# Kernel tuning notes

Hardware: AMD Instinct MI355X
Metric: run time of the kernel (lower is better)

## Reference

```python
import jax, jax.numpy as jnp
import numpy as np

SCOPE = 27
RICKER_WIDTH = 6.0
DAMPING = 0.12
IN_CHANNELS = 256


def _ricker(scope, std, damping):
    # mexican-hat / ricker wavelet, length `scope`, centered
    x = jnp.arange(scope, dtype=jnp.float32) - (scope // 2)
    a = 2.0 / (jnp.sqrt(3.0 * std) * jnp.pi ** 0.25)
    return damping * a * (1.0 - (x / std) ** 2) * jnp.exp(-(x ** 2) / (2.0 * std ** 2))


def _pad_roll(k, in_channels):
    # zero-pad kernel (length scope) to in_channels, roll so center sits at i=0-ish
    scope = k.shape[-1]
    pad_left = (in_channels - scope) // 2
    pad_right = in_channels - scope - pad_left
    padded = jnp.concatenate([jnp.zeros((pad_left,), k.dtype), k, jnp.zeros((pad_right,), k.dtype)])
    return jnp.roll(padded, in_channels // 2 + 1)


def _circulant(kernel, c):
    # tpl[i, j] = kernel[(j - i) mod C]  (each row is the kernel rolled by i)
    idx = (jnp.arange(c)[None, :] - jnp.arange(c)[:, None]) % c
    return kernel[idx]


def setup_inputs() -> dict:
    key = jax.random.key(0)
    k1, _ = jax.random.split(key)
    activations = jax.random.normal(k1, (32, IN_CHANNELS, 64, 64), dtype=jnp.float32)
    inhibition_filter = _ricker(SCOPE, RICKER_WIDTH, DAMPING)  # learned param, ricker init
    return {"activations": activations, "inhibition_filter": inhibition_filter}


def reference(activations, inhibition_filter):
    n, c, h, w = activations.shape
    kernel = _pad_roll(inhibition_filter, c)              # [C]
    tpl = _circulant(kernel, c)                           # [C, C]
    tpl_inv = jnp.linalg.inv(jnp.eye(c, dtype=tpl.dtype) - tpl)  # [C, C]
    # torch: (N, H*W, C) @ tpl_inv -> out[n, c_out, h, w] = sum_k act[n, k, h, w] * tpl_inv[k, c_out]
    return jnp.einsum('nkhw,kc->nchw', activations, tpl_inv)
```

## Files before the change

kernel.cpp:

```cpp
#include <hip/hip_runtime.h>
#include <hip/hip_bf16.h>

#define C 256
#define HW 4096
#define CHUNK_STRIDE 66

typedef __attribute__((ext_vector_type(8))) short short8;
typedef __attribute__((ext_vector_type(4))) float float4v;

__device__ __forceinline__ unsigned short f2bf(float x) {
    unsigned u = __builtin_bit_cast(unsigned, x);
    u = (u + 0x7fffu + ((u >> 16) & 1u)) >> 16;
    return (unsigned short)u;
}

__device__ __forceinline__ void g2l_b32(const void* g, void* l) {
    __builtin_amdgcn_global_load_lds(
        (const __attribute__((address_space(1))) unsigned int*)g,
        (__attribute__((address_space(3))) unsigned int*)l, 4, 0, 0);
}
__device__ __forceinline__ void g2l_b128(const void* g, void* l) {
    __builtin_amdgcn_global_load_lds(
        (const __attribute__((address_space(1))) unsigned int*)g,
        (__attribute__((address_space(3))) unsigned int*)l, 16, 0, 0);
}

__global__ void build_tab_kernel(const float* __restrict__ filt, unsigned short* __restrict__ tab) {
    __shared__ float twc[256], tws[256];
    __shared__ float Gre[256], Gim[256];
    __shared__ float gsh[256];
    const int t = threadIdx.x;
    const double PI = 3.14159265358979323846;
    double th = (double)t * (PI / 128.0);
    twc[t] = (float)cos(th);
    tws[t] = (float)sin(th);
    __syncthreads();
    float re = 1.0f, im = 0.0f;
    for (int i = 0; i < 27; ++i) {
        int d = (243 + i) & 255;
        int idx = (t * d) & 255;
        float fv = filt[i];
        re -= fv * twc[idx];
        im += fv * tws[idx];
    }
    float den = re * re + im * im;
    Gre[t] = re / den;
    Gim[t] = -im / den;
    __syncthreads();
    float acc = 0.0f;
    for (int f = 0; f < 256; ++f) {
        int idx = (f * t) & 255;
        acc += Gre[f] * twc[idx] - Gim[f] * tws[idx];
    }
    gsh[t] = acc * (1.0f / 256.0f);
    __syncthreads();
    for (int e = t; e < 16 * 64 * 8; e += 256) {
        int j = e & 7;
        int lane = (e >> 3) & 63;
        int s = e >> 9;
        int m = lane & 15, q = lane >> 4;
        int src = (m - 16 * s - 8 * q - j) & 255;
        tab[e] = f2bf(gsh[src]);
    }
}

__global__ __launch_bounds__(256, 3)
void toeplitz_gemm_kernel(const float* __restrict__ act,
                          const unsigned short* __restrict__ tab,
                          float* __restrict__ out) {
    __shared__ float chunkbuf[2][64 * CHUNK_STRIDE];
    __shared__ unsigned short afrags[16 * 64 * 8];

    const int tid = threadIdx.x;
    const int wave = tid >> 6;
    const int lane = tid & 63;
    const int m = lane & 15;
    const int quad = lane >> 4;
    const int blk = blockIdx.x;
    const int n = blk >> 6;
    const int p0 = (blk & 63) << 6;
    const float* actn = act + (size_t)n * (C * HW);
    float* outn = out + (size_t)n * (C * HW);

#pragma unroll
    for (int i = 0; i < 4; ++i) {
        const int seg = wave * 4 + i;
        g2l_b128(tab + seg * 512 + lane * 8, &afrags[seg * 512]);
    }

    {
        const float* src0 = actn + (size_t)(wave * 16) * HW + p0 + lane;
#pragma unroll
        for (int i = 0; i < 16; ++i)
            g2l_b32(src0 + (size_t)i * HW, &chunkbuf[0][(wave * 16 + i) * CHUNK_STRIDE]);
    }
    __syncthreads();

    float4v acc[4][4];
#pragma unroll
    for (int ct = 0; ct < 4; ++ct)
#pragma unroll
        for (int pt = 0; pt < 4; ++pt)
            acc[ct][pt] = (float4v){0.f, 0.f, 0.f, 0.f};

    for (int c = 0; c < 4; ++c) {
        if (c < 3) {
            const float* srcn = actn + (size_t)((c + 1) * 64 + wave * 16) * HW + p0 + lane;
#pragma unroll
            for (int i = 0; i < 16; ++i)
                g2l_b32(srcn + (size_t)i * HW, &chunkbuf[(c + 1) & 1][(wave * 16 + i) * CHUNK_STRIDE]);
        }

        const float* cb = chunkbuf[c & 1];
#pragma unroll
        for (int half = 0; half < 2; ++half) {
            const int ag = c * 2 + half;
            short8 bfr[4];
#pragma unroll
            for (int pt = 0; pt < 4; ++pt) {
                const float* base = cb + (half * 32 + quad * 8) * CHUNK_STRIDE + pt * 16 + m;
                unsigned u[8];
#pragma unroll
                for (int j = 0; j < 8; ++j)
                    u[j] = __builtin_bit_cast(unsigned, base[j * CHUNK_STRIDE]) + 0x8000u;
                uint4 pk;
                pk.x = (u[0] >> 16) | (u[1] & 0xFFFF0000u);
                pk.y = (u[2] >> 16) | (u[3] & 0xFFFF0000u);
                pk.z = (u[4] >> 16) | (u[5] & 0xFFFF0000u);
                pk.w = (u[6] >> 16) | (u[7] & 0xFFFF0000u);
                bfr[pt] = __builtin_bit_cast(short8, pk);
            }
#pragma unroll
            for (int ct = 0; ct < 4; ++ct) {
                const int sp = ((2 * ag - ct) - 4 * wave) & 15;
                const short8 af = *(const short8*)&afrags[sp * 512 + lane * 8];
#pragma unroll
                for (int pt = 0; pt < 4; ++pt)
                    acc[ct][pt] = __builtin_amdgcn_mfma_f32_16x16x32_bf16(
                        af, bfr[pt], acc[ct][pt], 0, 0, 0);
            }
        }
        if (c < 3) __syncthreads();
    }

#pragma unroll
    for (int ct = 0; ct < 4; ++ct) {
#pragma unroll
        for (int r = 0; r < 4; ++r) {
            const int cc = wave * 64 + ct * 16 + quad * 4 + r;
            float* op = outn + (size_t)cc * HW + p0;
#pragma unroll
            for (int pt = 0; pt < 4; ++pt) {
                op[pt * 16 + m] = acc[ct][pt][r];
            }
        }
    }
}

extern "C" void kernel_launch(void* const* d_in, const int* in_sizes, int n_in,
                              void* d_out, int out_size, void* d_ws, size_t ws_size,
                              hipStream_t stream) {
    const float* act = (const float*)d_in[0];
    const float* filt = (const float*)d_in[1];
    float* out = (float*)d_out;
    unsigned short* tab = (unsigned short*)d_ws;

    build_tab_kernel<<<1, 256, 0, stream>>>(filt, tab);
    toeplitz_gemm_kernel<<<2048, 256, 0, stream>>>(act, tab, out);
}
```

Baseline: 249.8 us.

## Load activations straight to registers with triple buffering, split waves by pixel

```diff
diff --git a/kernel.cpp b/kernel.cpp
--- a/kernel.cpp
+++ b/kernel.cpp
@@ -1,9 +1,7 @@
 #include <hip/hip_runtime.h>
-#include <hip/hip_bf16.h>
 
 #define C 256
 #define HW 4096
-#define CHUNK_STRIDE 66
 
 typedef __attribute__((ext_vector_type(8))) short short8;
 typedef __attribute__((ext_vector_type(4))) float float4v;
@@ -14,11 +12,6 @@
     return (unsigned short)u;
 }
 
-__device__ __forceinline__ void g2l_b32(const void* g, void* l) {
-    __builtin_amdgcn_global_load_lds(
-        (const __attribute__((address_space(1))) unsigned int*)g,
-        (__attribute__((address_space(3))) unsigned int*)l, 4, 0, 0);
-}
 __device__ __forceinline__ void g2l_b128(const void* g, void* l) {
     __builtin_amdgcn_global_load_lds(
         (const __attribute__((address_space(1))) unsigned int*)g,
@@ -58,17 +51,44 @@
         int j = e & 7;
         int lane = (e >> 3) & 63;
         int s = e >> 9;
-        int m = lane & 15, q = lane >> 4;
-        int src = (m - 16 * s - 8 * q - j) & 255;
+        int mm = lane & 15, q = lane >> 4;
+        int src = (mm - 16 * s - 8 * q - j) & 255;
         tab[e] = f2bf(gsh[src]);
     }
 }
 
-__global__ __launch_bounds__(256, 3)
+
+__device__ __forceinline__ void load8(unsigned (&u)[8], const float* __restrict__ base) {
+#pragma unroll
+    for (int j = 0; j < 8; ++j)
+        u[j] = __builtin_bit_cast(unsigned, base[j * HW]);
+}
+
+template <int AG>
+__device__ __forceinline__ void mfma_step(const unsigned (&u)[8],
+                                          const unsigned short* afrags,
+                                          int lane, float4v (&acc)[16]) {
+    unsigned v[8];
+#pragma unroll
+    for (int j = 0; j < 8; ++j) v[j] = u[j] + 0x8000u;
+    uint4 pk;
+    pk.x = (v[0] >> 16) | (v[1] & 0xFFFF0000u);
+    pk.y = (v[2] >> 16) | (v[3] & 0xFFFF0000u);
+    pk.z = (v[4] >> 16) | (v[5] & 0xFFFF0000u);
+    pk.w = (v[6] >> 16) | (v[7] & 0xFFFF0000u);
+    const short8 bfr = __builtin_bit_cast(short8, pk);
+#pragma unroll
+    for (int ct = 0; ct < 16; ++ct) {
+        const int sp = (2 * AG - ct) & 15;
+        const short8 af = *(const short8*)&afrags[sp * 512 + lane * 8];
+        acc[ct] = __builtin_amdgcn_mfma_f32_16x16x32_bf16(af, bfr, acc[ct], 0, 0, 0);
+    }
+}
+
+__global__ __launch_bounds__(256, 4)
 void toeplitz_gemm_kernel(const float* __restrict__ act,
                           const unsigned short* __restrict__ tab,
                           float* __restrict__ out) {
-    __shared__ float chunkbuf[2][64 * CHUNK_STRIDE];
     __shared__ unsigned short afrags[16 * 64 * 8];
 
     const int tid = threadIdx.x;
@@ -79,8 +99,8 @@
     const int blk = blockIdx.x;
     const int n = blk >> 6;
     const int p0 = (blk & 63) << 6;
-    const float* actn = act + (size_t)n * (C * HW);
-    float* outn = out + (size_t)n * (C * HW);
+    const float* __restrict__ actn = act + (size_t)n * (C * HW);
+    float* __restrict__ outn = out + (size_t)n * (C * HW);
 
 #pragma unroll
     for (int i = 0; i < 4; ++i) {
@@ -88,71 +108,39 @@
         g2l_b128(tab + seg * 512 + lane * 8, &afrags[seg * 512]);
     }
 
-    {
-        const float* src0 = actn + (size_t)(wave * 16) * HW + p0 + lane;
-#pragma unroll
-        for (int i = 0; i < 16; ++i)
-            g2l_b32(src0 + (size_t)i * HW, &chunkbuf[0][(wave * 16 + i) * CHUNK_STRIDE]);
-    }
+    const float* __restrict__ colp = actn + quad * 8 * HW + p0 + wave * 16 + m;
+
+    unsigned u0[8], u1[8], u2[8];
+    load8(u0, colp);
+    load8(u1, colp + 1 * 32 * HW);
+
     __syncthreads();
 
-    float4v acc[4][4];
+    float4v acc[16];
 #pragma unroll
-    for (int ct = 0; ct < 4; ++ct)
-#pragma unroll
-        for (int pt = 0; pt < 4; ++pt)
-            acc[ct][pt] = (float4v){0.f, 0.f, 0.f, 0.f};
+    for (int ct = 0; ct < 16; ++ct) acc[ct] = (float4v){0.f, 0.f, 0.f, 0.f};
 
-    for (int c = 0; c < 4; ++c) {
-        if (c < 3) {
-            const float* srcn = actn + (size_t)((c + 1) * 64 + wave * 16) * HW + p0 + lane;
-#pragma unroll
-            for (int i = 0; i < 16; ++i)
-                g2l_b32(srcn + (size_t)i * HW, &chunkbuf[(c + 1) & 1][(wave * 16 + i) * CHUNK_STRIDE]);
-        }
-
-        const float* cb = chunkbuf[c & 1];
-#pragma unroll
-        for (int half = 0; half < 2; ++half) {
-            const int ag = c * 2 + half;
-            short8 bfr[4];
-#pragma unroll
-            for (int pt = 0; pt < 4; ++pt) {
-                const float* base = cb + (half * 32 + quad * 8) * CHUNK_STRIDE + pt * 16 + m;
-                unsigned u[8];
-#pragma unroll
-                for (int j = 0; j < 8; ++j)
-                    u[j] = __builtin_bit_cast(unsigned, base[j * CHUNK_STRIDE]) + 0x8000u;
-                uint4 pk;
-                pk.x = (u[0] >> 16) | (u[1] & 0xFFFF0000u);
-                pk.y = (u[2] >> 16) | (u[3] & 0xFFFF0000u);
-                pk.z = (u[4] >> 16) | (u[5] & 0xFFFF0000u);
-                pk.w = (u[6] >> 16) | (u[7] & 0xFFFF0000u);
-                bfr[pt] = __builtin_bit_cast(short8, pk);
-            }
-#pragma unroll
-            for (int ct = 0; ct < 4; ++ct) {
-                const int sp = ((2 * ag - ct) - 4 * wave) & 15;
-                const short8 af = *(const short8*)&afrags[sp * 512 + lane * 8];
-#pragma unroll
-                for (int pt = 0; pt < 4; ++pt)
-                    acc[ct][pt] = __builtin_amdgcn_mfma_f32_16x16x32_bf16(
-                        af, bfr[pt], acc[ct][pt], 0, 0, 0);
-            }
-        }
-        if (c < 3) __syncthreads();
-    }
+    load8(u2, colp + 2 * 32 * HW);
+    mfma_step<0>(u0, afrags, lane, acc);
+    load8(u0, colp + 3 * 32 * HW);
+    mfma_step<1>(u1, afrags, lane, acc);
+    load8(u1, colp + 4 * 32 * HW);
+    mfma_step<2>(u2, afrags, lane, acc);
+    load8(u2, colp + 5 * 32 * HW);
+    mfma_step<3>(u0, afrags, lane, acc);
+    load8(u0, colp + 6 * 32 * HW);
+    mfma_step<4>(u1, afrags, lane, acc);
+    load8(u1, colp + 7 * 32 * HW);
+    mfma_step<5>(u2, afrags, lane, acc);
+    mfma_step<6>(u0, afrags, lane, acc);
+    mfma_step<7>(u1, afrags, lane, acc);
 
 #pragma unroll
-    for (int ct = 0; ct < 4; ++ct) {
+    for (int ct = 0; ct < 16; ++ct) {
 #pragma unroll
         for (int r = 0; r < 4; ++r) {
-            const int cc = wave * 64 + ct * 16 + quad * 4 + r;
-            float* op = outn + (size_t)cc * HW + p0;
-#pragma unroll
-            for (int pt = 0; pt < 4; ++pt) {
-                op[pt * 16 + m] = acc[ct][pt][r];
-            }
+            const int cc = ct * 16 + quad * 4 + r;
+            outn[(size_t)cc * HW + p0 + wave * 16 + m] = acc[ct][r];
         }
     }
 }
```

Result: slower. 390.3 us (+56.2%).

## Deepen activation prefetch to 4-buffer 32-row chunks with explicit vmcnt waits

Applied to the files above, without the earlier changes.

```diff
diff --git a/kernel.cpp b/kernel.cpp
--- a/kernel.cpp
+++ b/kernel.cpp
@@ -1,9 +1,11 @@
 #include <hip/hip_runtime.h>
-#include <hip/hip_bf16.h>
 
 #define C 256
 #define HW 4096
-#define CHUNK_STRIDE 66
+#define STRIDE 66
+#define CHROWS 32
+#define NCHUNK 8
+#define NBUF 4
 
 typedef __attribute__((ext_vector_type(8))) short short8;
 typedef __attribute__((ext_vector_type(4))) float float4v;
@@ -23,6 +25,12 @@
     __builtin_amdgcn_global_load_lds(
         (const __attribute__((address_space(1))) unsigned int*)g,
         (__attribute__((address_space(3))) unsigned int*)l, 16, 0, 0);
+}
+
+template <int N>
+__device__ __forceinline__ void wait_vmcnt() {
+    asm volatile("s_waitcnt vmcnt(%0)" :: "n"(N) : "memory");
+    __builtin_amdgcn_sched_barrier(0);
 }
 
 __global__ void build_tab_kernel(const float* __restrict__ filt, unsigned short* __restrict__ tab) {
@@ -58,8 +66,8 @@
         int j = e & 7;
         int lane = (e >> 3) & 63;
         int s = e >> 9;
-        int m = lane & 15, q = lane >> 4;
-        int src = (m - 16 * s - 8 * q - j) & 255;
+        int mm = lane & 15, q = lane >> 4;
+        int src = (mm - 16 * s - 8 * q - j) & 255;
         tab[e] = f2bf(gsh[src]);
     }
 }
@@ -68,7 +76,7 @@
 void toeplitz_gemm_kernel(const float* __restrict__ act,
                           const unsigned short* __restrict__ tab,
                           float* __restrict__ out) {
-    __shared__ float chunkbuf[2][64 * CHUNK_STRIDE];
+    __shared__ float chunkbuf[NBUF][CHROWS * STRIDE];
     __shared__ unsigned short afrags[16 * 64 * 8];
 
     const int tid = threadIdx.x;
@@ -79,8 +87,8 @@
     const int blk = blockIdx.x;
     const int n = blk >> 6;
     const int p0 = (blk & 63) << 6;
-    const float* actn = act + (size_t)n * (C * HW);
-    float* outn = out + (size_t)n * (C * HW);
+    const float* __restrict__ actn = act + (size_t)n * (C * HW);
+    float* __restrict__ outn = out + (size_t)n * (C * HW);
 
 #pragma unroll
     for (int i = 0; i < 4; ++i) {
@@ -88,13 +96,14 @@
         g2l_b128(tab + seg * 512 + lane * 8, &afrags[seg * 512]);
     }
 
-    {
-        const float* src0 = actn + (size_t)(wave * 16) * HW + p0 + lane;
+    auto issue = [&](int ch) {
+        const float* src = actn + (size_t)(ch * CHROWS + wave * 8) * HW + p0 + lane;
 #pragma unroll
-        for (int i = 0; i < 16; ++i)
-            g2l_b32(src0 + (size_t)i * HW, &chunkbuf[0][(wave * 16 + i) * CHUNK_STRIDE]);
-    }
-    __syncthreads();
+        for (int i = 0; i < 8; ++i)
+            g2l_b32(src + (size_t)i * HW, &chunkbuf[ch & (NBUF - 1)][(wave * 8 + i) * STRIDE]);
+    };
+
+    issue(0); issue(1); issue(2);
 
     float4v acc[4][4];
 #pragma unroll
@@ -103,45 +112,49 @@
         for (int pt = 0; pt < 4; ++pt)
             acc[ct][pt] = (float4v){0.f, 0.f, 0.f, 0.f};
 
-    for (int c = 0; c < 4; ++c) {
-        if (c < 3) {
-            const float* srcn = actn + (size_t)((c + 1) * 64 + wave * 16) * HW + p0 + lane;
-#pragma unroll
-            for (int i = 0; i < 16; ++i)
-                g2l_b32(srcn + (size_t)i * HW, &chunkbuf[(c + 1) & 1][(wave * 16 + i) * CHUNK_STRIDE]);
-        }
+#define PHASE(c, WN)                                                              \
+    {                                                                             \
+        wait_vmcnt<WN>();                                                         \
+        __builtin_amdgcn_s_barrier();                                             \
+        __builtin_amdgcn_sched_barrier(0);                                        \
+        asm volatile("" ::: "memory");                                            \
+        if ((c) + 3 < NCHUNK) issue((c) + 3);                                     \
+        const float* cb = &chunkbuf[(c) & (NBUF - 1)][0];                         \
+        short8 bfr[4];                                                            \
+        _Pragma("unroll")                                                         \
+        for (int pt = 0; pt < 4; ++pt) {                                          \
+            const float* base = cb + (quad * 8) * STRIDE + pt * 16 + m;           \
+            unsigned u[8];                                                        \
+            _Pragma("unroll")                                                     \
+            for (int j = 0; j < 8; ++j)                                           \
+                u[j] = __builtin_bit_cast(unsigned, base[j * STRIDE]) + 0x8000u;  \
+            uint4 pk;                                                             \
+            pk.x = (u[0] >> 16) | (u[1] & 0xFFFF0000u);                           \
+            pk.y = (u[2] >> 16) | (u[3] & 0xFFFF0000u);                           \
+            pk.z = (u[4] >> 16) | (u[5] & 0xFFFF0000u);                           \
+            pk.w = (u[6] >> 16) | (u[7] & 0xFFFF0000u);                           \
+            bfr[pt] = __builtin_bit_cast(short8, pk);                             \
+        }                                                                         \
+        _Pragma("unroll")                                                         \
+        for (int ct = 0; ct < 4; ++ct) {                                          \
+            const int sp = (2 * (c) - ct - 4 * wave) & 15;                        \
+            const short8 af = *(const short8*)&afrags[sp * 512 + lane * 8];       \
+            _Pragma("unroll")                                                     \
+            for (int pt = 0; pt < 4; ++pt)                                        \
+                acc[ct][pt] = __builtin_amdgcn_mfma_f32_16x16x32_bf16(            \
+                    af, bfr[pt], acc[ct][pt], 0, 0, 0);                           \
+        }                                                                         \
+    }
 
-        const float* cb = chunkbuf[c & 1];
-#pragma unroll
-        for (int half = 0; half < 2; ++half) {
-            const int ag = c * 2 + half;
-            short8 bfr[4];
-#pragma unroll
-            for (int pt = 0; pt < 4; ++pt) {
-                const float* base = cb + (half * 32 + quad * 8) * CHUNK_STRIDE + pt * 16 + m;
-                unsigned u[8];
-#pragma unroll
-                for (int j = 0; j < 8; ++j)
-                    u[j] = __builtin_bit_cast(unsigned, base[j * CHUNK_STRIDE]) + 0x8000u;
-                uint4 pk;
-                pk.x = (u[0] >> 16) | (u[1] & 0xFFFF0000u);
-                pk.y = (u[2] >> 16) | (u[3] & 0xFFFF0000u);
-                pk.z = (u[4] >> 16) | (u[5] & 0xFFFF0000u);
-                pk.w = (u[6] >> 16) | (u[7] & 0xFFFF0000u);
-                bfr[pt] = __builtin_bit_cast(short8, pk);
-            }
-#pragma unroll
-            for (int ct = 0; ct < 4; ++ct) {
-                const int sp = ((2 * ag - ct) - 4 * wave) & 15;
-                const short8 af = *(const short8*)&afrags[sp * 512 + lane * 8];
-#pragma unroll
-                for (int pt = 0; pt < 4; ++pt)
-                    acc[ct][pt] = __builtin_amdgcn_mfma_f32_16x16x32_bf16(
-                        af, bfr[pt], acc[ct][pt], 0, 0, 0);
-            }
-        }
-        if (c < 3) __syncthreads();
-    }
+    PHASE(0, 16)
+    PHASE(1, 16)
+    PHASE(2, 16)
+    PHASE(3, 16)
+    PHASE(4, 16)
+    PHASE(5, 16)
+    PHASE(6, 8)
+    PHASE(7, 0)
+#undef PHASE
 
 #pragma unroll
     for (int ct = 0; ct < 4; ++ct) {
```

After: 250.7 us. Within noise of the previous version (+0.4%).
